# Kernel tuning notes

Hardware: AMD Instinct MI355X
Metric: run time of the kernel (lower is better)

## Reference

```python
import jax, jax.numpy as jnp
import numpy as np

N = 50000          # n_nodes
E_RAND = 800000    # random edges (before self-loops)
D_FEAT = 128
ALPHA = 0.1
NITER = 10


def setup_inputs() -> dict:
    key = jax.random.key(0)
    k1, k2, k3 = jax.random.split(key, 3)
    r = jax.random.randint(k1, (E_RAND,), 0, N)
    c = jax.random.randint(k2, (E_RAND,), 0, N)
    loop = jnp.arange(N)
    # A + I  (self-loops appended, matching calc_A_hat's sp.eye addition)
    rows = jnp.concatenate([r, loop]).astype(jnp.int32)   # [850000]
    cols = jnp.concatenate([c, loop]).astype(jnp.int32)   # [850000]
    # D_vec = row sums of (A + I); symmetric normalization D^-1/2 (A+I) D^-1/2
    deg = jax.ops.segment_sum(jnp.ones(rows.shape[0], jnp.float32), rows, num_segments=N)
    dinv = 1.0 / jnp.sqrt(jnp.maximum(deg, 1.0))
    # A_hat values pre-scaled by (1 - alpha), as registered in the buffer
    vals = ((1.0 - ALPHA) * dinv[rows] * dinv[cols]).astype(jnp.float32)
    E = jax.random.normal(k3, (N, D_FEAT), dtype=jnp.float32)
    return {"E": E, "rows": rows, "cols": cols, "vals": vals}


def reference(E, rows, cols, vals):
    # preds_{t+1} = A_hat @ preds_t + alpha * E   (niter power-iteration steps)
    # spmm via gather + segment_sum over the COO edge list.
    def step(preds, _):
        msg = vals[:, None] * preds[cols]                       # [nnz, d]
        preds = jax.ops.segment_sum(msg, rows, num_segments=N) + ALPHA * E
        return preds, None
    out, _ = jax.lax.scan(step, E, None, length=NITER)
    return out
```

## Files before the change

kernel.cpp:

```cpp
#include <hip/hip_runtime.h>


#define ALPHA 0.1f
#define NITER 10
#define DFEAT 128
#define CHUNK 1024


__global__ void hist_rows(const int* __restrict__ rows, int* __restrict__ counts, int nnz) {
    int e = blockIdx.x * blockDim.x + threadIdx.x;
    if (e < nnz) atomicAdd(&counts[rows[e]], 1);
}

__global__ void scan_reduce(const int* __restrict__ counts, int* __restrict__ blockSums, int N) {
    __shared__ int lds[256];
    int b = blockIdx.x, t = threadIdx.x;
    int base = b * CHUNK + t * 4;
    int s = 0;
    if (base + 4 <= N) {
        int4 v = *(const int4*)(counts + base);
        s = v.x + v.y + v.z + v.w;
    } else {
        for (int k = 0; k < 4; ++k) if (base + k < N) s += counts[base + k];
    }
    lds[t] = s;
    __syncthreads();
    for (int off = 128; off > 0; off >>= 1) {
        if (t < off) lds[t] += lds[t + off];
        __syncthreads();
    }
    if (t == 0) blockSums[b] = lds[0];
}

__global__ void scan_blocksums(const int* __restrict__ blockSums, int* __restrict__ blockOff,
                               int* __restrict__ rowptr, int NB, int N) {
    __shared__ int lds[1024];
    int t = threadIdx.x;
    int v = (t < NB) ? blockSums[t] : 0;
    lds[t] = v;
    __syncthreads();
    for (int off = 1; off < 1024; off <<= 1) {
        int u = (t >= off) ? lds[t - off] : 0;
        __syncthreads();
        lds[t] += u;
        __syncthreads();
    }
    if (t < NB) blockOff[t] = (t == 0) ? 0 : lds[t - 1];
    if (t == 1023) rowptr[N] = lds[1023];
}

__global__ void scan_write(const int* __restrict__ counts, const int* __restrict__ blockOff,
                           int* __restrict__ rowptr, int* __restrict__ offs, int N) {
    __shared__ int lds[256];
    int b = blockIdx.x, t = threadIdx.x;
    int base = b * CHUNK + t * 4;
    int c0 = 0, c1 = 0, c2 = 0, c3 = 0;
    if (base + 4 <= N) {
        int4 v = *(const int4*)(counts + base);
        c0 = v.x; c1 = v.y; c2 = v.z; c3 = v.w;
    } else {
        if (base + 0 < N) c0 = counts[base + 0];
        if (base + 1 < N) c1 = counts[base + 1];
        if (base + 2 < N) c2 = counts[base + 2];
        if (base + 3 < N) c3 = counts[base + 3];
    }
    int s = c0 + c1 + c2 + c3;
    lds[t] = s;
    __syncthreads();
    for (int off = 1; off < 256; off <<= 1) {
        int u = (t >= off) ? lds[t - off] : 0;
        __syncthreads();
        lds[t] += u;
        __syncthreads();
    }
    int run = ((t == 0) ? 0 : lds[t - 1]) + blockOff[b];
    if (base + 0 < N) { rowptr[base + 0] = run; offs[base + 0] = run; run += c0; }
    if (base + 1 < N) { rowptr[base + 1] = run; offs[base + 1] = run; run += c1; }
    if (base + 2 < N) { rowptr[base + 2] = run; offs[base + 2] = run; run += c2; }
    if (base + 3 < N) { rowptr[base + 3] = run; offs[base + 3] = run; run += c3; }
}

__global__ void build_csr(const int* __restrict__ rows, const int* __restrict__ cols,
                          const float* __restrict__ vals, int* __restrict__ offsets,
                          int2* __restrict__ packed, int nnz) {
    int e = blockIdx.x * blockDim.x + threadIdx.x;
    if (e >= nnz) return;
    int r = rows[e];
    int pos = atomicAdd(&offsets[r], 1);
    int2 p;
    p.x = cols[e] << 8;
    p.y = __float_as_int(vals[e]);
    packed[pos] = p;
}


__device__ inline unsigned f32_to_bf16_rne(float f) {
    unsigned x = __float_as_uint(f);
    return (x + 0x7fffu + ((x >> 16) & 1u)) >> 16;
}

__global__ void cvt_f32_bf16(const float2* __restrict__ in, unsigned* __restrict__ out, int n2) {
    int i = blockIdx.x * blockDim.x + threadIdx.x;
    if (i < n2) {
        float2 v = in[i];
        out[i] = f32_to_bf16_rne(v.x) | (f32_to_bf16_rne(v.y) << 16);
    }
}


#define XPND(u)  __uint_as_float((u) << 16), __uint_as_float((u) & 0xffff0000u)

#define GACC(cofs, vbits)                                                         \
    {   uint4 x = *(const uint4*)(srcb + (size_t)(unsigned)(cofs) + soff);        \
        float v = __int_as_float(vbits);                                          \
        acc[0] += v * __uint_as_float(x.x << 16);                                 \
        acc[1] += v * __uint_as_float(x.x & 0xffff0000u);                         \
        acc[2] += v * __uint_as_float(x.y << 16);                                 \
        acc[3] += v * __uint_as_float(x.y & 0xffff0000u);                         \
        acc[4] += v * __uint_as_float(x.z << 16);                                 \
        acc[5] += v * __uint_as_float(x.z & 0xffff0000u);                         \
        acc[6] += v * __uint_as_float(x.w << 16);                                 \
        acc[7] += v * __uint_as_float(x.w & 0xffff0000u); }

template <bool DSTB>
__global__ void spmm_quad(const int* __restrict__ rowptr, const int2* __restrict__ packed,
                          const char* __restrict__ srcb, const char* __restrict__ Eb,
                          const float* __restrict__ Ef, void* __restrict__ dst, int N) {
    int wave = (blockIdx.x * blockDim.x + threadIdx.x) >> 6;
    int nwav = (gridDim.x * blockDim.x) >> 6;
    int lane = threadIdx.x & 63;
    int g    = lane >> 4;
    int sub  = lane & 15;
    const size_t soff = (size_t)sub * 16;

    for (int w4 = wave * 4; w4 < N; w4 += nwav * 4) {
        int w = w4 + g;
        if (w >= N) w = N - 1;
        bool valid = (w4 + g < N);

        int s = rowptr[w];
        int e = rowptr[w + 1];

        float acc[8];
        if constexpr (DSTB) {
            uint4 ev = *(const uint4*)(Eb + (size_t)w * 256 + soff);
            acc[0] = ALPHA * __uint_as_float(ev.x << 16);
            acc[1] = ALPHA * __uint_as_float(ev.x & 0xffff0000u);
            acc[2] = ALPHA * __uint_as_float(ev.y << 16);
            acc[3] = ALPHA * __uint_as_float(ev.y & 0xffff0000u);
            acc[4] = ALPHA * __uint_as_float(ev.z << 16);
            acc[5] = ALPHA * __uint_as_float(ev.z & 0xffff0000u);
            acc[6] = ALPHA * __uint_as_float(ev.w << 16);
            acc[7] = ALPHA * __uint_as_float(ev.w & 0xffff0000u);
        } else {
            const float4* ep = (const float4*)(Ef + (size_t)w * DFEAT + sub * 8);
            float4 e0 = ep[0], e1 = ep[1];
            acc[0] = ALPHA * e0.x; acc[1] = ALPHA * e0.y;
            acc[2] = ALPHA * e0.z; acc[3] = ALPHA * e0.w;
            acc[4] = ALPHA * e1.x; acc[5] = ALPHA * e1.y;
            acc[6] = ALPHA * e1.z; acc[7] = ALPHA * e1.w;
        }

        int i = s;
        if (i < e && (i & 1)) {
            int2 p = packed[i];
            GACC(p.x, p.y)
            ++i;
        }
        for (; i + 4 <= e; i += 4) {
            int4 q0 = *(const int4*)(packed + i);
            int4 q1 = *(const int4*)(packed + i + 2);
            GACC(q0.x, q0.y)
            GACC(q0.z, q0.w)
            GACC(q1.x, q1.y)
            GACC(q1.z, q1.w)
        }
        for (; i < e; ++i) {
            int2 p = packed[i];
            GACC(p.x, p.y)
        }

        if (valid) {
            if constexpr (DSTB) {
                uint4 o;
                o.x = f32_to_bf16_rne(acc[0]) | (f32_to_bf16_rne(acc[1]) << 16);
                o.y = f32_to_bf16_rne(acc[2]) | (f32_to_bf16_rne(acc[3]) << 16);
                o.z = f32_to_bf16_rne(acc[4]) | (f32_to_bf16_rne(acc[5]) << 16);
                o.w = f32_to_bf16_rne(acc[6]) | (f32_to_bf16_rne(acc[7]) << 16);
                *(uint4*)((char*)dst + (size_t)w * 256 + soff) = o;
            } else {
                float4* op = (float4*)((float*)dst + (size_t)w * DFEAT + sub * 8);
                op[0] = make_float4(acc[0], acc[1], acc[2], acc[3]);
                op[1] = make_float4(acc[4], acc[5], acc[6], acc[7]);
            }
        }
    }
}

#undef GACC
#undef XPND

extern "C" void kernel_launch(void* const* d_in, const int* in_sizes, int n_in,
                              void* d_out, int out_size, void* d_ws, size_t ws_size,
                              hipStream_t stream) {
    const float* E    = (const float*)d_in[0];
    const int*   rows = (const int*)d_in[1];
    const int*   cols = (const int*)d_in[2];
    const float* vals = (const float*)d_in[3];
    float*       out  = (float*)d_out;

    const int nd  = in_sizes[0];
    const int nnz = in_sizes[1];
    const int N   = nd / DFEAT;
    const int NB  = (N + CHUNK - 1) / CHUNK;

    const int Np  = (N + 4 + 3) & ~3;
    const int NBp = (NB + 3) & ~3;
    char* ws = (char*)d_ws;
    char*  bufA    = ws;
    char*  bufB    = ws + (size_t)nd * 2;
    int*   rowptr  = (int*)(ws + (size_t)nd * 4);
    int*   offs    = rowptr + Np;
    int*   bsums   = offs + Np;
    int*   boff    = bsums + NBp;
    size_t pk_off  = (((size_t)nd * 4 + (size_t)(2 * Np + 2 * NBp) * 4) + 15) & ~(size_t)15;
    int2*  packed  = (int2*)(ws + pk_off);

    char* Eb = (char*)d_out;

    dim3 blk(256);
    dim3 gE((nnz + 255) / 256);

    hipMemsetAsync(offs, 0, (size_t)N * 4, stream);
    hist_rows<<<gE, blk, 0, stream>>>(rows, offs, nnz);
    scan_reduce<<<NB, 256, 0, stream>>>(offs, bsums, N);
    scan_blocksums<<<1, 1024, 0, stream>>>(bsums, boff, rowptr, NB, N);
    scan_write<<<NB, 256, 0, stream>>>(offs, boff, rowptr, offs, N);
    build_csr<<<gE, blk, 0, stream>>>(rows, cols, vals, offs, packed, nnz);

    const int n2 = nd / 2;
    cvt_f32_bf16<<<(n2 + 255) / 256, blk, 0, stream>>>((const float2*)E, (unsigned*)Eb, n2);

    int quads  = (N + 3) / 4;
    int waves  = (quads + 1) / 2;
    int blocks = (waves + 3) / 4;
    dim3 gS(blocks);

    char* cur = Eb;
    char* nxt = bufA;
    for (int it = 1; it <= NITER - 1; ++it) {
        spmm_quad<true><<<gS, blk, 0, stream>>>(rowptr, packed, cur, Eb, E, nxt, N);
        cur = nxt;
        nxt = (cur == bufA) ? bufB : bufA;
    }
    spmm_quad<false><<<gS, blk, 0, stream>>>(rowptr, packed, cur, Eb, E, out, N);
}
```

Before: 440.7 us.

## Split SpMM feature dimension into two half-width passes with eight rows per wave

Each SpMM iteration now runs as two launches, each covering 64 of the 128 feature columns. A wave processes eight rows with eight lanes each instead of four rows with sixteen lanes. Each launch gathers only half of every source row, so its working set is half the size and may fit better in cache. In exchange, the CSR index/value stream and rowptr are read twice per iteration, and the number of kernel launches doubles.

```diff
diff --git a/kernel.cpp b/kernel.cpp
--- a/kernel.cpp
+++ b/kernel.cpp
@@ -108,8 +108,6 @@
 }
 
 
-#define XPND(u)  __uint_as_float((u) << 16), __uint_as_float((u) & 0xffff0000u)
-
 #define GACC(cofs, vbits)                                                         \
     {   uint4 x = *(const uint4*)(srcb + (size_t)(unsigned)(cofs) + soff);        \
         float v = __int_as_float(vbits);                                          \
@@ -123,20 +121,21 @@
         acc[7] += v * __uint_as_float(x.w & 0xffff0000u); }
 
 template <bool DSTB>
-__global__ void spmm_quad(const int* __restrict__ rowptr, const int2* __restrict__ packed,
-                          const char* __restrict__ srcb, const char* __restrict__ Eb,
-                          const float* __restrict__ Ef, void* __restrict__ dst, int N) {
+__global__ void spmm_oct(const int* __restrict__ rowptr, const int2* __restrict__ packed,
+                         const char* __restrict__ srcb, const char* __restrict__ Eb,
+                         const float* __restrict__ Ef, void* __restrict__ dst,
+                         int N, int pf) {
     int wave = (blockIdx.x * blockDim.x + threadIdx.x) >> 6;
     int nwav = (gridDim.x * blockDim.x) >> 6;
     int lane = threadIdx.x & 63;
-    int g    = lane >> 4;
-    int sub  = lane & 15;
-    const size_t soff = (size_t)sub * 16;
-
-    for (int w4 = wave * 4; w4 < N; w4 += nwav * 4) {
-        int w = w4 + g;
+    int g    = lane >> 3;
+    int sub  = lane & 7;
+    const size_t soff = (size_t)pf * 2 + (size_t)sub * 16;
+
+    for (int w8 = wave * 8; w8 < N; w8 += nwav * 8) {
+        int w = w8 + g;
         if (w >= N) w = N - 1;
-        bool valid = (w4 + g < N);
+        bool valid = (w8 + g < N);
 
         int s = rowptr[w];
         int e = rowptr[w + 1];
@@ -153,7 +152,7 @@
             acc[6] = ALPHA * __uint_as_float(ev.w << 16);
             acc[7] = ALPHA * __uint_as_float(ev.w & 0xffff0000u);
         } else {
-            const float4* ep = (const float4*)(Ef + (size_t)w * DFEAT + sub * 8);
+            const float4* ep = (const float4*)(Ef + (size_t)w * DFEAT + pf + sub * 8);
             float4 e0 = ep[0], e1 = ep[1];
             acc[0] = ALPHA * e0.x; acc[1] = ALPHA * e0.y;
             acc[2] = ALPHA * e0.z; acc[3] = ALPHA * e0.w;
@@ -189,7 +188,7 @@
                 o.w = f32_to_bf16_rne(acc[6]) | (f32_to_bf16_rne(acc[7]) << 16);
                 *(uint4*)((char*)dst + (size_t)w * 256 + soff) = o;
             } else {
-                float4* op = (float4*)((float*)dst + (size_t)w * DFEAT + sub * 8);
+                float4* op = (float4*)((float*)dst + (size_t)w * DFEAT + pf + sub * 8);
                 op[0] = make_float4(acc[0], acc[1], acc[2], acc[3]);
                 op[1] = make_float4(acc[4], acc[5], acc[6], acc[7]);
             }
@@ -198,7 +197,6 @@
 }
 
 #undef GACC
-#undef XPND
 
 extern "C" void kernel_launch(void* const* d_in, const int* in_sizes, int n_in,
                               void* d_out, int out_size, void* d_ws, size_t ws_size,
@@ -241,17 +239,18 @@
     const int n2 = nd / 2;
     cvt_f32_bf16<<<(n2 + 255) / 256, blk, 0, stream>>>((const float2*)E, (unsigned*)Eb, n2);
 
-    int quads  = (N + 3) / 4;
-    int waves  = (quads + 1) / 2;
-    int blocks = (waves + 3) / 4;
+    int octs   = (N + 7) / 8;
+    int blocks = (octs + 3) / 4;
     dim3 gS(blocks);
 
     char* cur = Eb;
     char* nxt = bufA;
     for (int it = 1; it <= NITER - 1; ++it) {
-        spmm_quad<true><<<gS, blk, 0, stream>>>(rowptr, packed, cur, Eb, E, nxt, N);
+        spmm_oct<true><<<gS, blk, 0, stream>>>(rowptr, packed, cur, Eb, E, nxt, N, 0);
+        spmm_oct<true><<<gS, blk, 0, stream>>>(rowptr, packed, cur, Eb, E, nxt, N, 64);
         cur = nxt;
         nxt = (cur == bufA) ? bufB : bufA;
     }
-    spmm_quad<false><<<gS, blk, 0, stream>>>(rowptr, packed, cur, Eb, E, out, N);
-}
+    spmm_oct<false><<<gS, blk, 0, stream>>>(rowptr, packed, cur, Eb, E, out, N, 0);
+    spmm_oct<false><<<gS, blk, 0, stream>>>(rowptr, packed, cur, Eb, E, out, N, 64);
+}
```

Result: slower. 454.1 us (+3.0%).

## Build CSR via two-pass bucketed scatter instead of global per-row atomics

Applied to the files above, without the earlier changes.

Replaces the single-pass CSR build, which does a global atomicAdd per edge on a per-row cursor, with a two-pass bucket sort. Pass A groups edges into 256-row buckets using LDS histograms and one global atomic per bucket per block, writing to a staging buffer. Pass B places each bucket's edges at their final positions using LDS atomics. The aim is fewer global atomics and more local writes during setup. The cost is an extra pass over the edges and a staging buffer that reuses bufA. It also depends on N being small enough for at most 256 buckets. A possible race exists: scan_write writes bucket cursors into the same array it reads counts from.

```diff
diff --git a/kernel.cpp b/kernel.cpp
--- a/kernel.cpp
+++ b/kernel.cpp
@@ -5,6 +5,7 @@
 #define NITER 10
 #define DFEAT 128
 #define CHUNK 1024
+#define EPB   4096
 
 
 __global__ void hist_rows(const int* __restrict__ rows, int* __restrict__ counts, int nnz) {
@@ -50,7 +51,7 @@
 }
 
 __global__ void scan_write(const int* __restrict__ counts, const int* __restrict__ blockOff,
-                           int* __restrict__ rowptr, int* __restrict__ offs, int N) {
+                           int* __restrict__ rowptr, int* __restrict__ bucketCursor, int N) {
     __shared__ int lds[256];
     int b = blockIdx.x, t = threadIdx.x;
     int base = b * CHUNK + t * 4;
@@ -74,23 +75,77 @@
         __syncthreads();
     }
     int run = ((t == 0) ? 0 : lds[t - 1]) + blockOff[b];
-    if (base + 0 < N) { rowptr[base + 0] = run; offs[base + 0] = run; run += c0; }
-    if (base + 1 < N) { rowptr[base + 1] = run; offs[base + 1] = run; run += c1; }
-    if (base + 2 < N) { rowptr[base + 2] = run; offs[base + 2] = run; run += c2; }
-    if (base + 3 < N) { rowptr[base + 3] = run; offs[base + 3] = run; run += c3; }
-}
-
-__global__ void build_csr(const int* __restrict__ rows, const int* __restrict__ cols,
-                          const float* __restrict__ vals, int* __restrict__ offsets,
-                          int2* __restrict__ packed, int nnz) {
-    int e = blockIdx.x * blockDim.x + threadIdx.x;
-    if (e >= nnz) return;
-    int r = rows[e];
-    int pos = atomicAdd(&offsets[r], 1);
-    int2 p;
-    p.x = cols[e] << 8;
-    p.y = __float_as_int(vals[e]);
-    packed[pos] = p;
+    #pragma unroll
+    for (int k = 0; k < 4; ++k) {
+        int r = base + k;
+        if (r < N) {
+            rowptr[r] = run;
+            if ((r & 255) == 0) bucketCursor[r >> 8] = run;
+            run += (k == 0 ? c0 : k == 1 ? c1 : k == 2 ? c2 : c3);
+        }
+    }
+}
+
+__global__ void csr_bucketA(const int* __restrict__ rows, const int* __restrict__ cols,
+                            const float* __restrict__ vals, int* __restrict__ bucketCursor,
+                            int2* __restrict__ staging, int nnz, int nbuck) {
+    __shared__ int h[256], base[256], cur[256];
+    const int t = threadIdx.x;
+    const int e0 = blockIdx.x * EPB;
+
+    if (t < 256) { h[t] = 0; cur[t] = 0; }
+    __syncthreads();
+
+    #pragma unroll
+    for (int k = 0; k < EPB / 256; ++k) {
+        int idx = e0 + k * 256 + t;
+        if (idx < nnz) atomicAdd(&h[rows[idx] >> 8], 1);
+    }
+    __syncthreads();
+
+    if (t < 256 && t < nbuck && h[t] > 0)
+        base[t] = atomicAdd(&bucketCursor[t], h[t]);
+    __syncthreads();
+
+    #pragma unroll
+    for (int k = 0; k < EPB / 256; ++k) {
+        int idx = e0 + k * 256 + t;
+        if (idx < nnz) {
+            int r = rows[idx];
+            int b = r >> 8;
+            int o = atomicAdd(&cur[b], 1);
+            int2 p;
+            p.x = (cols[idx] << 8) | (r & 255);
+            p.y = __float_as_int(vals[idx]);
+            staging[base[b] + o] = p;
+        }
+    }
+}
+
+__global__ void csr_bucketB(const int* __restrict__ rowptr, const int2* __restrict__ staging,
+                            int2* __restrict__ packed, int N) {
+    __shared__ int cur[256];
+    const int b = blockIdx.x;
+    const int t = threadIdx.x;
+    const int r0 = b << 8;
+
+    int rlim = r0 + t;
+    cur[t] = rowptr[rlim < N ? rlim : N];
+    __syncthreads();
+
+    const int s0 = rowptr[r0];
+    int r1 = r0 + 256;
+    const int s1 = rowptr[r1 < N ? r1 : N];
+
+    for (int idx = s0 + t; idx < s1; idx += 256) {
+        int2 e = staging[idx];
+        int rl = e.x & 255;
+        int pos = atomicAdd(&cur[rl], 1);
+        int2 p;
+        p.x = e.x & 0xffffff00;
+        p.y = e.y;
+        packed[pos] = p;
+    }
 }
 
 
@@ -107,8 +162,6 @@
     }
 }
 
-
-#define XPND(u)  __uint_as_float((u) << 16), __uint_as_float((u) & 0xffff0000u)
 
 #define GACC(cofs, vbits)                                                         \
     {   uint4 x = *(const uint4*)(srcb + (size_t)(unsigned)(cofs) + soff);        \
@@ -198,7 +251,6 @@
 }
 
 #undef GACC
-#undef XPND
 
 extern "C" void kernel_launch(void* const* d_in, const int* in_sizes, int n_in,
                               void* d_out, int out_size, void* d_ws, size_t ws_size,
@@ -213,6 +265,7 @@
     const int nnz = in_sizes[1];
     const int N   = nd / DFEAT;
     const int NB  = (N + CHUNK - 1) / CHUNK;
+    const int nbuck = (N + 255) >> 8;
 
     const int Np  = (N + 4 + 3) & ~3;
     const int NBp = (NB + 3) & ~3;
@@ -220,23 +273,26 @@
     char*  bufA    = ws;
     char*  bufB    = ws + (size_t)nd * 2;
     int*   rowptr  = (int*)(ws + (size_t)nd * 4);
-    int*   offs    = rowptr + Np;
-    int*   bsums   = offs + Np;
+    int*   bcur    = rowptr + Np;
+    int*   bsums   = bcur + Np;
     int*   boff    = bsums + NBp;
     size_t pk_off  = (((size_t)nd * 4 + (size_t)(2 * Np + 2 * NBp) * 4) + 15) & ~(size_t)15;
     int2*  packed  = (int2*)(ws + pk_off);
+    int2*  staging = (int2*)bufA;
 
     char* Eb = (char*)d_out;
 
     dim3 blk(256);
     dim3 gE((nnz + 255) / 256);
 
-    hipMemsetAsync(offs, 0, (size_t)N * 4, stream);
-    hist_rows<<<gE, blk, 0, stream>>>(rows, offs, nnz);
-    scan_reduce<<<NB, 256, 0, stream>>>(offs, bsums, N);
+    hipMemsetAsync(bcur, 0, (size_t)N * 4, stream);
+    hist_rows<<<gE, blk, 0, stream>>>(rows, bcur, nnz);
+    scan_reduce<<<NB, 256, 0, stream>>>(bcur, bsums, N);
     scan_blocksums<<<1, 1024, 0, stream>>>(bsums, boff, rowptr, NB, N);
-    scan_write<<<NB, 256, 0, stream>>>(offs, boff, rowptr, offs, N);
-    build_csr<<<gE, blk, 0, stream>>>(rows, cols, vals, offs, packed, nnz);
+    scan_write<<<NB, 256, 0, stream>>>(bcur, boff, rowptr, bcur, N);
+    csr_bucketA<<<(nnz + EPB - 1) / EPB, blk, 0, stream>>>(rows, cols, vals, bcur,
+                                                           staging, nnz, nbuck);
+    csr_bucketB<<<nbuck, blk, 0, stream>>>(rowptr, staging, packed, N);
 
     const int n2 = nd / 2;
     cvt_f32_bf16<<<(n2 + 255) / 256, blk, 0, stream>>>((const float2*)E, (unsigned*)Eb, n2);
```

Result: faster. 416.6 us, median of 2 (-5.5%).
